# Kernel tuning notes

Hardware: AMD Instinct MI355X
Metric: run time of the kernel (lower is better)

Reference implementation:

```python
import jax, jax.numpy as jnp
import numpy as np
from jax import lax

B, S, E, H = 4, 1024, 512, 8
D = E // H


def setup_inputs() -> dict:
    key = jax.random.key(0)
    k1, k2, k3 = jax.random.split(key, 3)
    source = jax.random.normal(k1, (B, S, E), dtype=jnp.float32)
    target = jax.random.normal(k2, (B, S, E), dtype=jnp.float32)
    # orthogonal-initialized positional encoder [1, H, 1, D]; random rows are a fine stand-in
    enc = jax.random.normal(k3, (1, H, 1, D), dtype=jnp.float32)
    enc = enc / jnp.linalg.norm(enc, axis=-1, keepdims=True)
    return {
        "source": source,
        "target": target,
        "encoder": enc,
        "alpha": jnp.float32(1.0),
        "beta": jnp.float32(1.0),
        "gamma": jnp.float32(2.0),
    }


def _split_heads(x):
    b, s, e = x.shape
    return x.reshape(b, s, H, e // H).transpose(0, 2, 1, 3)  # [B,H,S,D]


def reference(source, target, encoder, alpha, beta, gamma):
    q = _split_heads(source)  # [B,H,S,D]
    k = _split_heads(target)  # [B,H,S,D]
    pe = encoder[0, :, 0, :]  # [H,D]

    # --- grammar (time) attention: sequential tanh recurrence over t ---
    def step(cc, k_t):
        # cc, k_t: [B,H,D]
        cc = jnp.tanh(cc * pe)
        out = jnp.einsum('bhsd,bhd->bhs', q, cc)  # [B,H,S]
        return k_t * cc, out  # decay_rate = 0.0

    cc0 = k[:, :, 0, :]                      # initial cumulative context
    k_ts = jnp.moveaxis(k, 2, 0)             # [S,B,H,D]
    _, outs = lax.scan(step, cc0, k_ts)      # outs: [S,B,H,S]
    grammar = jnp.moveaxis(outs, 0, 3) / jnp.sqrt(jnp.float32(D))  # [B,H,S,S]
    grammar = jax.nn.softmax(grammar, axis=-1)

    # --- semantic attention ---
    semantic = jnp.einsum('bhsd,bhtd->bhst', q, k) / 100.0  # [B,H,S,S]

    w = jax.nn.softmax((alpha * semantic + beta * grammar) / gamma, axis=-1)

    # merge_heads: [B,H,S,S] -> [B,S,H*S]
    wm = w.transpose(0, 2, 1, 3).reshape(B, S, H * S)
    # output: wm^T @ target -> [B, H*S, E]
    return jnp.matmul(wm.transpose(0, 2, 1), target)
```

## Files before the change

kernel.cpp:

```cpp
#include <hip/hip_runtime.h>
#include <hip/hip_bf16.h>
#include <stdint.h>

#define S_LEN 1024
#define E_DIM 512
#define H_NUM 8
#define D_DIM 64
#define B_NUM 4
#define BH_NUM 32

using s16x8 = __attribute__((ext_vector_type(8))) short;
using f32x4 = __attribute__((ext_vector_type(4))) float;
using us4   = __attribute__((ext_vector_type(4))) unsigned short;

typedef const __attribute__((address_space(1))) uint32_t gas_uint;
typedef __attribute__((address_space(3))) uint32_t las_uint;

static __device__ __forceinline__ unsigned short f2bf(float f) {
  __hip_bfloat16 h = __float2bfloat16(f);
  return __builtin_bit_cast(unsigned short, h);
}
static __device__ __forceinline__ float bf2f(unsigned short u) {
  return __bfloat162float(__builtin_bit_cast(__hip_bfloat16, u));
}

#define NB_RECUR 8
#define NB_PACK  2048
#define NB_TR    512

__global__ __launch_bounds__(256) void k_prep(const float* __restrict__ src,
                                              const float* __restrict__ tgt,
                                              const float* __restrict__ enc,
                                              __hip_bfloat16* __restrict__ qb,
                                              __hip_bfloat16* __restrict__ kb,
                                              __hip_bfloat16* __restrict__ cb,
                                              __hip_bfloat16* __restrict__ tT) {
  __shared__ float tile[64][65];
  const int bid = blockIdx.x;
  const int tid = threadIdx.x;

  if (bid < NB_RECUR) {
    int g = bid * 256 + tid;
    int d = g & 63;
    int bh = g >> 6;
    int h = bh & 7;
    int b = bh >> 3;
    float pe = enc[h * D_DIM + d];
    float pe2 = 2.0f * pe;
    const float* tp = tgt + (size_t)b * S_LEN * E_DIM + h * D_DIM + d;
    __hip_bfloat16* cp = cb + (size_t)bh * S_LEN * D_DIM + d;

    constexpr int CH = 32;
    float bufA[CH], bufB[CH];
#pragma unroll
    for (int i = 0; i < CH; ++i) bufA[i] = tp[(size_t)i * E_DIM];
    float cc = bufA[0];

#pragma unroll 1
    for (int ch = 0; ch < S_LEN / CH; ch += 2) {
      if (ch + 1 < S_LEN / CH) {
#pragma unroll
        for (int i = 0; i < CH; ++i)
          bufB[i] = tp[(size_t)((ch + 1) * CH + i) * E_DIM];
      }
#pragma unroll
      for (int i = 0; i < CH; ++i) {
        float m = cc * pe2;
        float e = __expf(-fabsf(m));
        float th = __builtin_copysignf((1.0f - e) * __builtin_amdgcn_rcpf(1.0f + e), m);
        cp[(size_t)(ch * CH + i) * D_DIM] = __float2bfloat16(th);
        cc = bufA[i] * th;
      }
      if (ch + 2 < S_LEN / CH) {
#pragma unroll
        for (int i = 0; i < CH; ++i)
          bufA[i] = tp[(size_t)((ch + 2) * CH + i) * E_DIM];
      }
#pragma unroll
      for (int i = 0; i < CH; ++i) {
        float m = cc * pe2;
        float e = __expf(-fabsf(m));
        float th = __builtin_copysignf((1.0f - e) * __builtin_amdgcn_rcpf(1.0f + e), m);
        cp[(size_t)((ch + 1) * CH + i) * D_DIM] = __float2bfloat16(th);
        cc = bufB[i] * th;
      }
    }
  } else if (bid < NB_RECUR + NB_PACK) {
    size_t i4 = ((size_t)(bid - NB_RECUR) * 256 + tid) * 4;
    float4 s4 = *reinterpret_cast<const float4*>(src + i4);
    float4 t4 = *reinterpret_cast<const float4*>(tgt + i4);
    int e = (int)(i4 & 511);
    size_t bs = i4 >> 9;
    int s = (int)(bs & 1023);
    int b = (int)(bs >> 10);
    int h = e >> 6, d = e & 63;
    size_t o = (((size_t)(b * H_NUM + h) * S_LEN) + s) * D_DIM + d;
    us4 qv = {f2bf(s4.x), f2bf(s4.y), f2bf(s4.z), f2bf(s4.w)};
    us4 kv = {f2bf(t4.x), f2bf(t4.y), f2bf(t4.z), f2bf(t4.w)};
    *reinterpret_cast<us4*>(qb + o) = qv;
    *reinterpret_cast<us4*>(kb + o) = kv;
  } else {
    int lb = bid - (NB_RECUR + NB_PACK);
    int sx = lb & 15, ey = (lb >> 4) & 7, b = lb >> 7;
    int e0 = ey * 64, s0 = sx * 64;
    int tx = tid & 63, ty = tid >> 6;
    const float* p = tgt + ((size_t)b * S_LEN + s0) * E_DIM + e0;
#pragma unroll
    for (int r = ty; r < 64; r += 4) tile[r][tx] = p[(size_t)r * E_DIM + tx];
    __syncthreads();
    __hip_bfloat16* q = tT + ((size_t)b * E_DIM + e0) * S_LEN + s0;
#pragma unroll
    for (int r = ty; r < 64; r += 4) q[(size_t)r * S_LEN + tx] = __float2bfloat16(tile[tx][r]);
  }
}

__global__ __launch_bounds__(256) void k_weights(const __hip_bfloat16* __restrict__ qb,
                                                 const __hip_bfloat16* __restrict__ kb,
                                                 const __hip_bfloat16* __restrict__ cb,
                                                 __hip_bfloat16* __restrict__ wt,
                                                 const float* __restrict__ pal,
                                                 const float* __restrict__ pbe,
                                                 const float* __restrict__ pga) {
  __shared__ unsigned short stage[4][4][2048];
  __shared__ float red0[4][16];
  __shared__ float red1[4][16];

  const int tid = threadIdx.x;
  const int wave = tid >> 6, lane = tid & 63;
  const int quad = lane >> 4, col = lane & 15;

  const int g = blockIdx.x;
  const int xcd = g & 7;
  const int r = g >> 3;
  const int bh = xcd * 4 + (r >> 6);
  const int s0 = (r & 63) * 16;

  const float alpha = pal[0], beta = pbe[0];
  const float inv_gamma = 1.0f / pga[0];
  const float sa = alpha * 0.01f * inv_gamma;
  const float sb = beta * inv_gamma;

  const __hip_bfloat16* qrow = qb + ((size_t)bh * S_LEN + s0 + col) * D_DIM;
  s16x8 a0 = *reinterpret_cast<const s16x8*>(qrow + quad * 8);
  s16x8 a1 = *reinterpret_cast<const s16x8*>(qrow + 32 + quad * 8);

  const int t_base = wave * 256;
  uint32_t stg[16][2];
  float    stk[16][4];

  const char* cbase = (const char*)(cb + ((size_t)bh * S_LEN + t_base) * D_DIM);
  const char* kbase = (const char*)(kb + ((size_t)bh * S_LEN + t_base) * D_DIM);
  const int so0 = ((lane >> 3) << 7) | (((lane & 7) ^ ((lane >> 3) & 7)) << 4);

  auto stage_it = [&](int it) {
    unsigned short* db = &stage[wave][it & 3][0];
    const char* cs = cbase + it * 2048;
    const char* ks = kbase + it * 2048;
    __builtin_amdgcn_global_load_lds((gas_uint*)(cs + so0),        (las_uint*)(db),        16, 0, 0);
    __builtin_amdgcn_global_load_lds((gas_uint*)(cs + so0 + 1024), (las_uint*)(db + 512),  16, 0, 0);
    __builtin_amdgcn_global_load_lds((gas_uint*)(ks + so0),        (las_uint*)(db + 1024), 16, 0, 0);
    __builtin_amdgcn_global_load_lds((gas_uint*)(ks + so0 + 1024), (las_uint*)(db + 1536), 16, 0, 0);
  };

  const int xswz = (col & 7) << 4;
  const int rb = col * 128;

  s16x8 cF0[2], cF1[2], kF0[2], kF1[2];

  stage_it(0);
  stage_it(1);
  stage_it(2);
  asm volatile("s_waitcnt vmcnt(8)" ::: "memory");
  {
    const char* cw = (const char*)&stage[wave][0][0];
    const char* kw = cw + 2048;
    cF0[0] = *reinterpret_cast<const s16x8*>(cw + rb + ((quad * 16) ^ xswz));
    cF1[0] = *reinterpret_cast<const s16x8*>(cw + rb + ((64 + quad * 16) ^ xswz));
    kF0[0] = *reinterpret_cast<const s16x8*>(kw + rb + ((quad * 16) ^ xswz));
    kF1[0] = *reinterpret_cast<const s16x8*>(kw + rb + ((64 + quad * 16) ^ xswz));
  }

  float lg[4] = {0.f, 0.f, 0.f, 0.f};
#pragma unroll
  for (int it = 0; it < 16; ++it) {
    if (it + 3 < 16) stage_it(it + 3);
    if (it < 13)       asm volatile("s_waitcnt vmcnt(8)" ::: "memory");
    else if (it == 13) asm volatile("s_waitcnt vmcnt(4)" ::: "memory");
    else if (it == 14) asm volatile("s_waitcnt vmcnt(0)" ::: "memory");
    if (it < 15) {
      const char* cw = (const char*)&stage[wave][(it + 1) & 3][0];
      const char* kw = cw + 2048;
      const int sl = (it + 1) & 1;
      cF0[sl] = *reinterpret_cast<const s16x8*>(cw + rb + ((quad * 16) ^ xswz));
      cF1[sl] = *reinterpret_cast<const s16x8*>(cw + rb + ((64 + quad * 16) ^ xswz));
      kF0[sl] = *reinterpret_cast<const s16x8*>(kw + rb + ((quad * 16) ^ xswz));
      kF1[sl] = *reinterpret_cast<const s16x8*>(kw + rb + ((64 + quad * 16) ^ xswz));
    }
    const int cur = it & 1;
    f32x4 dg = {0.f, 0.f, 0.f, 0.f};
    f32x4 dk = {0.f, 0.f, 0.f, 0.f};
    __builtin_amdgcn_s_setprio(1);
    dg = __builtin_amdgcn_mfma_f32_16x16x32_bf16(a0, cF0[cur], dg, 0, 0, 0);
    dg = __builtin_amdgcn_mfma_f32_16x16x32_bf16(a1, cF1[cur], dg, 0, 0, 0);
    dk = __builtin_amdgcn_mfma_f32_16x16x32_bf16(a0, kF0[cur], dk, 0, 0, 0);
    dk = __builtin_amdgcn_mfma_f32_16x16x32_bf16(a1, kF1[cur], dk, 0, 0, 0);
    __builtin_amdgcn_s_setprio(0);
    uint32_t p0 = 0, p1 = 0;
#pragma unroll
    for (int i = 0; i < 4; ++i) {
      float gv = __expf(dg[i] * 0.125f);
      unsigned short u = f2bf(gv);
      lg[i] += bf2f(u);
      if (i < 2) p0 |= (uint32_t)u << (16 * i);
      else       p1 |= (uint32_t)u << (16 * (i - 2));
      stk[it][i] = dk[i];
    }
    stg[it][0] = p0;
    stg[it][1] = p1;
  }
#pragma unroll
  for (int m = 1; m < 16; m <<= 1) {
#pragma unroll
    for (int i = 0; i < 4; ++i) lg[i] += __shfl_xor(lg[i], m);
  }
  if (col == 0) {
#pragma unroll
    for (int i = 0; i < 4; ++i) red0[wave][quad * 4 + i] = lg[i];
  }
  __syncthreads();
  float ilg[4];
#pragma unroll
  for (int i = 0; i < 4; ++i) {
    int rr = quad * 4 + i;
    ilg[i] = 1.0f / (red0[0][rr] + red0[1][rr] + red0[2][rr] + red0[3][rr]);
  }

  float lw[4] = {0.f, 0.f, 0.f, 0.f};
#pragma unroll
  for (int it = 0; it < 16; ++it) {
#pragma unroll
    for (int i = 0; i < 4; ++i) {
      unsigned short u = (unsigned short)((i < 2 ? stg[it][0] >> (16 * i)
                                                 : stg[it][1] >> (16 * (i - 2))) & 0xffffu);
      float gv = bf2f(u) * ilg[i];
      float z = sa * stk[it][i] + sb * gv;
      float wv = __expf(z);
      stk[it][i] = wv;
      lw[i] += wv;
    }
  }
#pragma unroll
  for (int m = 1; m < 16; m <<= 1) {
#pragma unroll
    for (int i = 0; i < 4; ++i) lw[i] += __shfl_xor(lw[i], m);
  }
  if (col == 0) {
#pragma unroll
    for (int i = 0; i < 4; ++i) red1[wave][quad * 4 + i] = lw[i];
  }
  __syncthreads();
  float ilw[4];
#pragma unroll
  for (int i = 0; i < 4; ++i) {
    int rr = quad * 4 + i;
    ilw[i] = 1.0f / (red1[0][rr] + red1[1][rr] + red1[2][rr] + red1[3][rr]);
  }

  __hip_bfloat16* wrow = wt + ((size_t)bh * S_LEN + t_base + col) * S_LEN + s0 + quad * 4;
#pragma unroll
  for (int it = 0; it < 16; ++it) {
    us4 o;
#pragma unroll
    for (int i = 0; i < 4; ++i) o[i] = f2bf(stk[it][i] * ilw[i]);
    *reinterpret_cast<us4*>(wrow + (size_t)it * 16 * S_LEN) = o;
  }
}

__global__ __launch_bounds__(256) void k_outgemm(const __hip_bfloat16* __restrict__ wt,
                                                 const __hip_bfloat16* __restrict__ tT,
                                                 float* __restrict__ out) {
  __shared__ __hip_bfloat16 As[2][128 * 64];
  __shared__ __hip_bfloat16 Bs[2][128 * 64];
  const int tid = threadIdx.x;
  const int wave = tid >> 6, lane = tid & 63;
  const int quad = lane >> 4, col = lane & 15;

  const int g = blockIdx.x;
  const int xcd = g & 7;
  const int local = g >> 3;
  const int strip = xcd * 32 + (local >> 2);
  const int ntile = local & 3;
  const int bh = strip >> 3;
  const int mt = strip & 7;
  const int b = bh >> 3;
  const int m0 = mt * 128;
  const int n0 = ntile * 128;

  const __hip_bfloat16* Ag = wt + (size_t)bh * S_LEN * S_LEN;
  const __hip_bfloat16* Bg = tT + (size_t)b * E_DIM * S_LEN;
  const int mw = (wave >> 1) * 64, nw = (wave & 1) * 64;
  const int lrow = lane >> 3;
  const int lcolswz = ((lane & 7) ^ lrow) * 8;

  f32x4 acc[4][4];
#pragma unroll
  for (int i = 0; i < 4; ++i)
#pragma unroll
    for (int j = 0; j < 4; ++j) acc[i][j] = (f32x4){0.f, 0.f, 0.f, 0.f};

  auto stage = [&](int kt, int buf) {
    const int k0 = kt * 64;
#pragma unroll
    for (int j = 0; j < 4; ++j) {
      const int rbase = j * 32 + wave * 8;
      const __hip_bfloat16* gpA = Ag + (size_t)(m0 + rbase + lrow) * S_LEN + k0 + lcolswz;
      __builtin_amdgcn_global_load_lds((gas_uint*)gpA,
                                       (las_uint*)(&As[buf][rbase * 64]), 16, 0, 0);
      const __hip_bfloat16* gpB = Bg + (size_t)(n0 + rbase + lrow) * S_LEN + k0 + lcolswz;
      __builtin_amdgcn_global_load_lds((gas_uint*)gpB,
                                       (las_uint*)(&Bs[buf][rbase * 64]), 16, 0, 0);
    }
  };

  const int swz = (col & 7) << 4;
  auto compute = [&](int buf) {
    const char* Ab = (const char*)&As[buf][0];
    const char* Bb = (const char*)&Bs[buf][0];
    __builtin_amdgcn_s_setprio(1);
#pragma unroll
    for (int ks = 0; ks < 2; ++ks) {
      s16x8 af[4], bfr[4];
#pragma unroll
      for (int i = 0; i < 4; ++i)
        af[i] = *reinterpret_cast<const s16x8*>(
            Ab + (size_t)(mw + i * 16 + col) * 128 + ((ks * 64 + quad * 16) ^ swz));
#pragma unroll
      for (int i = 0; i < 4; ++i)
        bfr[i] = *reinterpret_cast<const s16x8*>(
            Bb + (size_t)(nw + i * 16 + col) * 128 + ((ks * 64 + quad * 16) ^ swz));
#pragma unroll
      for (int mi = 0; mi < 4; ++mi)
#pragma unroll
        for (int ni = 0; ni < 4; ++ni)
          acc[mi][ni] = __builtin_amdgcn_mfma_f32_16x16x32_bf16(af[mi], bfr[ni], acc[mi][ni], 0, 0, 0);
    }
    __builtin_amdgcn_s_setprio(0);
  };

  stage(0, 0);
#pragma unroll 1
  for (int kt = 0; kt < 15; ++kt) {
    stage(kt + 1, (kt + 1) & 1);
    asm volatile("s_waitcnt vmcnt(8)" ::: "memory");
    __builtin_amdgcn_s_barrier();
    compute(kt & 1);
    asm volatile("" ::: "memory");
    __builtin_amdgcn_s_barrier();
  }
  asm volatile("s_waitcnt vmcnt(0)" ::: "memory");
  __builtin_amdgcn_s_barrier();
  compute(1);

#pragma unroll
  for (int mi = 0; mi < 4; ++mi)
#pragma unroll
    for (int ni = 0; ni < 4; ++ni)
#pragma unroll
      for (int i = 0; i < 4; ++i) {
        int m = m0 + mw + mi * 16 + quad * 4 + i;
        int n = n0 + nw + ni * 16 + col;
        out[((size_t)bh * S_LEN + m) * E_DIM + n] = acc[mi][ni][i];
      }
}

extern "C" void kernel_launch(void* const* d_in, const int* in_sizes, int n_in,
                              void* d_out, int out_size, void* d_ws, size_t ws_size,
                              hipStream_t stream) {
  (void)in_sizes; (void)n_in; (void)out_size; (void)ws_size;
  const float* src = (const float*)d_in[0];
  const float* tgt = (const float*)d_in[1];
  const float* enc = (const float*)d_in[2];
  const float* pal = (const float*)d_in[3];
  const float* pbe = (const float*)d_in[4];
  const float* pga = (const float*)d_in[5];
  float* out = (float*)d_out;

  char* ws = (char*)d_ws;
  __hip_bfloat16* qb = (__hip_bfloat16*)(ws);
  __hip_bfloat16* kb = (__hip_bfloat16*)(ws + ((size_t)4 << 20));
  __hip_bfloat16* cb = (__hip_bfloat16*)(ws + ((size_t)8 << 20));
  __hip_bfloat16* tT = (__hip_bfloat16*)(ws + ((size_t)12 << 20));
  __hip_bfloat16* wt = (__hip_bfloat16*)(ws + ((size_t)16 << 20));

  k_prep<<<NB_RECUR + NB_PACK + NB_TR, 256, 0, stream>>>(src, tgt, enc, qb, kb, cb, tT);
  k_weights<<<dim3((S_LEN / 16) * BH_NUM), 256, 0, stream>>>(qb, kb, cb, wt, pal, pbe, pga);
  k_outgemm<<<dim3((E_DIM / 128) * (S_LEN / 128) * BH_NUM), 256, 0, stream>>>(wt, tT, out);
}
```

Before: 204.8 us.

## Enlarge output GEMM tiles to 256x256 with 8 waves and 4-stage pipeline

Rewrites the final weights-times-target GEMM to use 256x256 block tiles with 512 threads, K steps of 32 and a 4-deep LDS ring buffer. A and B loads are interleaved between the two MFMA half-phases. Grid drops from 1024 to 256 blocks. Larger tiles halve global re-reads of the big bf16 weight matrix and deepen prefetch, but each wave now holds 128 accumulator registers and there are fewer blocks to spread across CUs.

```diff
diff --git a/kernel.cpp b/kernel.cpp
--- a/kernel.cpp
+++ b/kernel.cpp
@@ -276,11 +276,11 @@
   }
 }
 
-__global__ __launch_bounds__(256) void k_outgemm(const __hip_bfloat16* __restrict__ wt,
+__global__ __launch_bounds__(512) void k_outgemm(const __hip_bfloat16* __restrict__ wt,
                                                  const __hip_bfloat16* __restrict__ tT,
                                                  float* __restrict__ out) {
-  __shared__ __hip_bfloat16 As[2][128 * 64];
-  __shared__ __hip_bfloat16 Bs[2][128 * 64];
+  __shared__ __hip_bfloat16 As[4][256 * 32];
+  __shared__ __hip_bfloat16 Bs[4][256 * 32];
   const int tid = threadIdx.x;
   const int wave = tid >> 6, lane = tid & 63;
   const int quad = lane >> 4, col = lane & 15;
@@ -288,88 +288,102 @@
   const int g = blockIdx.x;
   const int xcd = g & 7;
   const int local = g >> 3;
-  const int strip = xcd * 32 + (local >> 2);
-  const int ntile = local & 3;
-  const int bh = strip >> 3;
-  const int mt = strip & 7;
+  const int bh = xcd * 4 + (local >> 3);
+  const int tile = local & 7;
+  const int m0 = (tile >> 1) * 256;
+  const int n0 = (tile & 1) * 256;
   const int b = bh >> 3;
-  const int m0 = mt * 128;
-  const int n0 = ntile * 128;
 
   const __hip_bfloat16* Ag = wt + (size_t)bh * S_LEN * S_LEN;
   const __hip_bfloat16* Bg = tT + (size_t)b * E_DIM * S_LEN;
-  const int mw = (wave >> 1) * 64, nw = (wave & 1) * 64;
-  const int lrow = lane >> 3;
-  const int lcolswz = ((lane & 7) ^ lrow) * 8;
-
-  f32x4 acc[4][4];
-#pragma unroll
-  for (int i = 0; i < 4; ++i)
+
+  const int mw = (wave >> 2) * 128;
+  const int nw = (wave & 3) * 64;
+
+  const int scol  = ((lane & 3) ^ ((lane >> 3) & 3)) * 8;
+  const int sslot = (quad ^ ((col >> 1) & 3)) * 16;
+
+  f32x4 acc[8][4];
+#pragma unroll
+  for (int i = 0; i < 8; ++i)
 #pragma unroll
     for (int j = 0; j < 4; ++j) acc[i][j] = (f32x4){0.f, 0.f, 0.f, 0.f};
 
-  auto stage = [&](int kt, int buf) {
-    const int k0 = kt * 64;
-#pragma unroll
-    for (int j = 0; j < 4; ++j) {
-      const int rbase = j * 32 + wave * 8;
-      const __hip_bfloat16* gpA = Ag + (size_t)(m0 + rbase + lrow) * S_LEN + k0 + lcolswz;
-      __builtin_amdgcn_global_load_lds((gas_uint*)gpA,
-                                       (las_uint*)(&As[buf][rbase * 64]), 16, 0, 0);
-      const __hip_bfloat16* gpB = Bg + (size_t)(n0 + rbase + lrow) * S_LEN + k0 + lcolswz;
-      __builtin_amdgcn_global_load_lds((gas_uint*)gpB,
-                                       (las_uint*)(&Bs[buf][rbase * 64]), 16, 0, 0);
+  auto stageA = [&](int kt) {
+    const int k0 = kt * 32;
+    __hip_bfloat16* L = &As[kt & 3][0];
+#pragma unroll
+    for (int j = 0; j < 2; ++j) {
+      const int R = j * 128 + wave * 16 + (lane >> 2);
+      const __hip_bfloat16* gp = Ag + (size_t)(m0 + R) * S_LEN + k0 + scol;
+      __builtin_amdgcn_global_load_lds((gas_uint*)gp,
+                                       (las_uint*)(L + (j * 128 + wave * 16) * 32), 16, 0, 0);
     }
   };
-
-  const int swz = (col & 7) << 4;
-  auto compute = [&](int buf) {
-    const char* Ab = (const char*)&As[buf][0];
-    const char* Bb = (const char*)&Bs[buf][0];
-    __builtin_amdgcn_s_setprio(1);
-#pragma unroll
-    for (int ks = 0; ks < 2; ++ks) {
+  auto stageB = [&](int kt) {
+    const int k0 = kt * 32;
+    __hip_bfloat16* L = &Bs[kt & 3][0];
+#pragma unroll
+    for (int j = 0; j < 2; ++j) {
+      const int R = j * 128 + wave * 16 + (lane >> 2);
+      const __hip_bfloat16* gp = Bg + (size_t)(n0 + R) * S_LEN + k0 + scol;
+      __builtin_amdgcn_global_load_lds((gas_uint*)gp,
+                                       (las_uint*)(L + (j * 128 + wave * 16) * 32), 16, 0, 0);
+    }
+  };
+
+  stageA(0); stageB(0); stageA(1); stageB(1);
+  asm volatile("s_waitcnt vmcnt(4)" ::: "memory");
+  __builtin_amdgcn_s_barrier();
+
+#pragma unroll 1
+  for (int kt = 0; kt < 32; ++kt) {
+    const char* Ab = (const char*)&As[kt & 3][0];
+    const char* Bb = (const char*)&Bs[kt & 3][0];
+#pragma unroll
+    for (int p = 0; p < 2; ++p) {
       s16x8 af[4], bfr[4];
 #pragma unroll
-      for (int i = 0; i < 4; ++i)
-        af[i] = *reinterpret_cast<const s16x8*>(
-            Ab + (size_t)(mw + i * 16 + col) * 128 + ((ks * 64 + quad * 16) ^ swz));
-#pragma unroll
-      for (int i = 0; i < 4; ++i)
-        bfr[i] = *reinterpret_cast<const s16x8*>(
-            Bb + (size_t)(nw + i * 16 + col) * 128 + ((ks * 64 + quad * 16) ^ swz));
+      for (int i = 0; i < 4; ++i) {
+        const int row = mw + (p * 4 + i) * 16 + col;
+        af[i] = *reinterpret_cast<const s16x8*>(Ab + row * 64 + sslot);
+      }
+#pragma unroll
+      for (int i = 0; i < 4; ++i) {
+        const int row = nw + i * 16 + col;
+        bfr[i] = *reinterpret_cast<const s16x8*>(Bb + row * 64 + sslot);
+      }
+      if (kt + 2 < 32) {
+        if (p == 0) stageA(kt + 2);
+        else        stageB(kt + 2);
+      }
+      __builtin_amdgcn_s_barrier();
+      asm volatile("s_waitcnt lgkmcnt(0)" ::: "memory");
+      __builtin_amdgcn_s_setprio(1);
 #pragma unroll
       for (int mi = 0; mi < 4; ++mi)
 #pragma unroll
         for (int ni = 0; ni < 4; ++ni)
-          acc[mi][ni] = __builtin_amdgcn_mfma_f32_16x16x32_bf16(af[mi], bfr[ni], acc[mi][ni], 0, 0, 0);
-    }
-    __builtin_amdgcn_s_setprio(0);
-  };
-
-  stage(0, 0);
-#pragma unroll 1
-  for (int kt = 0; kt < 15; ++kt) {
-    stage(kt + 1, (kt + 1) & 1);
-    asm volatile("s_waitcnt vmcnt(8)" ::: "memory");
-    __builtin_amdgcn_s_barrier();
-    compute(kt & 1);
-    asm volatile("" ::: "memory");
-    __builtin_amdgcn_s_barrier();
-  }
-  asm volatile("s_waitcnt vmcnt(0)" ::: "memory");
-  __builtin_amdgcn_s_barrier();
-  compute(1);
-
-#pragma unroll
-  for (int mi = 0; mi < 4; ++mi)
-#pragma unroll
-    for (int ni = 0; ni < 4; ++ni)
+          acc[p * 4 + mi][ni] = __builtin_amdgcn_mfma_f32_16x16x32_bf16(
+              af[mi], bfr[ni], acc[p * 4 + mi][ni], 0, 0, 0);
+      __builtin_amdgcn_s_setprio(0);
+      if (p == 1) {
+        if (kt < 30)       asm volatile("s_waitcnt vmcnt(4)" ::: "memory");
+        else if (kt == 30) asm volatile("s_waitcnt vmcnt(0)" ::: "memory");
+      }
+      __builtin_amdgcn_s_barrier();
+    }
+  }
+
+#pragma unroll
+  for (int mf = 0; mf < 8; ++mf)
+#pragma unroll
+    for (int nf = 0; nf < 4; ++nf)
 #pragma unroll
       for (int i = 0; i < 4; ++i) {
-        int m = m0 + mw + mi * 16 + quad * 4 + i;
-        int n = n0 + nw + ni * 16 + col;
-        out[((size_t)bh * S_LEN + m) * E_DIM + n] = acc[mi][ni][i];
+        int m = m0 + mw + mf * 16 + quad * 4 + i;
+        int n = n0 + nw + nf * 16 + col;
+        out[((size_t)bh * S_LEN + m) * E_DIM + n] = acc[mf][nf][i];
       }
 }
 
@@ -394,5 +408,5 @@
 
   k_prep<<<NB_RECUR + NB_PACK + NB_TR, 256, 0, stream>>>(src, tgt, enc, qb, kb, cb, tT);
   k_weights<<<dim3((S_LEN / 16) * BH_NUM), 256, 0, stream>>>(qb, kb, cb, wt, pal, pbe, pga);
-  k_outgemm<<<dim3((E_DIM / 128) * (S_LEN / 128) * BH_NUM), 256, 0, stream>>>(wt, tT, out);
-}
+  k_outgemm<<<dim3(256), 512, 0, stream>>>(wt, tT, out);
+}
```

Result: no change. 202.2 us (-1.2%).
